# Kernel optimization log

Hardware: AMD Instinct MI355X
Metric: run time of the kernel (lower is better)

## Reference

```python
import jax, jax.numpy as jnp
import numpy as np

B, H, E = 1024, 2048, 1024

def _xavier(key, shape):
    # torch xavier_normal_ on [1, out, in]: std = sqrt(2/(fan_in+fan_out)) over last two dims
    fan_out, fan_in = shape[-2], shape[-1]
    std = (2.0 / (fan_in + fan_out)) ** 0.5
    return jax.random.normal(key, shape, jnp.float32) * std

def setup_inputs() -> dict:
    key = jax.random.key(0)
    ks = jax.random.split(key, 17)
    inp = {
        'x': jax.random.normal(ks[0], (B, E, 1), jnp.float32),
        'c': jax.random.normal(ks[1], (B, H, 1), jnp.float32),
        'h': jax.random.normal(ks[2], (B, H, 1), jnp.float32),
        'W_xi': _xavier(ks[3], (1, H, E)), 'W_hi': _xavier(ks[4], (1, H, H)), 'B_i': _xavier(ks[5], (1, H, 1)),
        'W_xg': _xavier(ks[6], (1, H, E)), 'W_hg': _xavier(ks[7], (1, H, H)), 'B_g': _xavier(ks[8], (1, H, 1)),
        'W_xf': _xavier(ks[9], (1, H, E)), 'W_hf': _xavier(ks[10], (1, H, H)), 'B_f': _xavier(ks[11], (1, H, 1)),
        'W_xo': _xavier(ks[12], (1, H, E)), 'W_ho': _xavier(ks[13], (1, H, H)), 'B_o': _xavier(ks[14], (1, H, 1)),
        'W_hy': _xavier(ks[15], (1, E, H)), 'B_y': _xavier(ks[16], (1, E, 1)),
    }
    return inp

def reference(x, c, h, W_xi, W_hi, B_i, W_xg, W_hg, B_g, W_xf, W_hf, B_f, W_xo, W_ho, B_o, W_hy, B_y):
    # jnp.matmul broadcasts the leading batch dim: [1,H,E] @ [B,E,1] -> [B,H,1]
    i = jax.nn.sigmoid(jnp.matmul(W_xi, x) + jnp.matmul(W_hi, h) + B_i)
    g = jnp.tanh(jnp.matmul(W_xg, x) + jnp.matmul(W_hg, h) + B_g)
    f = jax.nn.sigmoid(jnp.matmul(W_xf, x) + jnp.matmul(W_hf, h) + B_f)
    c_new = f * c + i * g
    o = jax.nn.sigmoid(jnp.matmul(W_xo, x) + jnp.matmul(W_ho, h) + B_o)
    h_new = o * c_new  # NOTE: source uses o*c (no tanh), faithful to original
    y = jnp.tanh(jnp.matmul(W_hy, h_new) + B_y)
    return (y, c_new, h_new)
```

## Files before the change

kernel.cpp:

```cpp
#include <hip/hip_runtime.h>

#define B_SZ 1024
#define H_SZ 2048
#define E_SZ 1024

typedef float  f32x4 __attribute__((ext_vector_type(4)));
typedef short  s16x8 __attribute__((ext_vector_type(8)));

__device__ __forceinline__ unsigned short f2bf(float f) {
    unsigned u = __float_as_uint(f);
    u = u + 0x7fffu + ((u >> 16) & 1u);
    return (unsigned short)(u >> 16);
}
__device__ __forceinline__ float bf2f(unsigned short s) {
    return __uint_as_float(((unsigned)s) << 16);
}
__device__ __forceinline__ float sigm(float v) {
    return 1.0f / (1.0f + __expf(-v));
}

__device__ __forceinline__ void gll(const unsigned short* g, unsigned short* l) {
    __builtin_amdgcn_global_load_lds(
        (const __attribute__((address_space(1))) unsigned int*)g,
        (__attribute__((address_space(3))) unsigned int*)l, 16, 0, 0);
}

struct CastArgs {
    const float*    src[11];
    unsigned short* dst[11];
    int             n[11];
};

__global__ __launch_bounds__(256) void cast_kernel(CastArgs a) {
    const int arr = blockIdx.y;
    const int n = a.n[arr];
    const float* __restrict__ s = a.src[arr];
    unsigned short* __restrict__ d = a.dst[arr];
    const int stride = gridDim.x * 256 * 4;
    for (int i = (blockIdx.x * 256 + threadIdx.x) * 4; i < n; i += stride) {
        float4 v = *(const float4*)(s + i);
        ushort4 o;
        o.x = f2bf(v.x); o.y = f2bf(v.y); o.z = f2bf(v.z); o.w = f2bf(v.w);
        *(ushort4*)(d + i) = o;
    }
}

__device__ __forceinline__ void gemm_accum64(
    const unsigned short* __restrict__ A,
    const unsigned short* __restrict__ W,
    int ld, int kLen, int m0, int n0,
    unsigned short* lA, unsigned short* lB,
    f32x4 acc[4][4], int t)
{
    const int lane = t & 63;
    const int w    = t >> 6;
    const int wr   = (w >> 1) << 6;
    const int wc   = (w & 1) << 6;
    const int lr   = lane & 15;
    const int q4   = lane >> 4;

    const int srow = t >> 3;
    const int scol = ((t & 7) ^ (srow & 7)) << 3;
    const unsigned short* gA = A + (size_t)(m0 + srow) * ld + scol;
    const unsigned short* gB = W + (size_t)(n0 + srow) * ld + scol;
    const size_t st32 = (size_t)32 * ld;

    const int cb0 = ((q4    ) ^ (lr & 7)) << 3;
    const int cb1 = ((4 + q4) ^ (lr & 7)) << 3;

    for (int k0 = 0; k0 < kLen; k0 += 64) {
#pragma unroll
        for (int p = 0; p < 4; ++p)
            gll(gA + k0 + p * st32, lA + (t + 256 * p) * 8);
#pragma unroll
        for (int p = 0; p < 4; ++p)
            gll(gB + k0 + p * st32, lB + (t + 256 * p) * 8);
        __syncthreads();

#pragma unroll
        for (int ks = 0; ks < 2; ++ks) {
            const int cb = ks ? cb1 : cb0;
            s16x8 af[4], bfr[4];
#pragma unroll
            for (int i = 0; i < 4; ++i)
                af[i] = *(const s16x8*)(lA + (wr + i * 16 + lr) * 64 + cb);
#pragma unroll
            for (int j = 0; j < 4; ++j)
                bfr[j] = *(const s16x8*)(lB + (wc + j * 16 + lr) * 64 + cb);
#pragma unroll
            for (int i = 0; i < 4; ++i)
#pragma unroll
                for (int j = 0; j < 4; ++j)
                    acc[i][j] = __builtin_amdgcn_mfma_f32_16x16x32_bf16(
                        af[i], bfr[j], acc[i][j], 0, 0, 0);
        }
        __syncthreads();
    }
}

__global__ __launch_bounds__(256) void gates_kernel(
    const unsigned short* __restrict__ Xb,
    const unsigned short* __restrict__ Hb,
    const unsigned short* __restrict__ Wxb,
    const unsigned short* __restrict__ Whb,
    const float* __restrict__ bi, const float* __restrict__ bg,
    const float* __restrict__ bff, const float* __restrict__ bo,
    unsigned short* __restrict__ Z)
{
    __shared__ unsigned short lA[128 * 64];
    __shared__ unsigned short lB[128 * 64];
    const int t   = threadIdx.x;
    const int b   = blockIdx.x;
    const int xcd = b & 7;
    const int i_  = b >> 3;
    const int nt  = xcd * 8 + (i_ >> 3);
    const int m0  = (i_ & 7) * 128;
    const int q   = nt >> 4;
    const int n0  = (nt & 15) * 128;

    f32x4 acc[4][4] = {};
    gemm_accum64(Xb, Wxb + (size_t)q * H_SZ * E_SZ, E_SZ, E_SZ, m0, n0, lA, lB, acc, t);
    gemm_accum64(Hb, Whb + (size_t)q * H_SZ * H_SZ, H_SZ, H_SZ, m0, n0, lA, lB, acc, t);

    const float* bias = (q == 0) ? bi : (q == 1) ? bg : (q == 2) ? bff : bo;
    const int lane = t & 63, w = t >> 6;
    const int wr = (w >> 1) << 6, wc = (w & 1) << 6;
    const int lr = lane & 15, rq = (lane >> 4) << 2;
    unsigned short* Zq = Z + (size_t)q * B_SZ * H_SZ;
#pragma unroll
    for (int i = 0; i < 4; ++i) {
#pragma unroll
        for (int j = 0; j < 4; ++j) {
            const int n = n0 + wc + j * 16 + lr;
            const float bv = bias[n];
#pragma unroll
            for (int r = 0; r < 4; ++r) {
                const int m = m0 + wr + i * 16 + rq + r;
                const float v = acc[i][j][r] + bv;
                const float a = (q == 1) ? tanhf(v) : sigm(v);
                Zq[(size_t)m * H_SZ + n] = f2bf(a);
            }
        }
    }
}

__global__ __launch_bounds__(256) void cell_kernel(
    const unsigned short* __restrict__ Z, const float* __restrict__ c,
    float* __restrict__ c_out, float* __restrict__ h_out,
    unsigned short* __restrict__ HnB)
{
    const size_t BH = (size_t)B_SZ * H_SZ;
    const int idx = (blockIdx.x * 256 + threadIdx.x) * 4;
    ushort4 iu = *(const ushort4*)(Z + idx);
    ushort4 gu = *(const ushort4*)(Z + BH + idx);
    ushort4 fu = *(const ushort4*)(Z + 2 * BH + idx);
    ushort4 ou = *(const ushort4*)(Z + 3 * BH + idx);
    float4 cv = *(const float4*)(c + idx);

    float cn[4], hn[4];
    cn[0] = bf2f(fu.x) * cv.x + bf2f(iu.x) * bf2f(gu.x);
    cn[1] = bf2f(fu.y) * cv.y + bf2f(iu.y) * bf2f(gu.y);
    cn[2] = bf2f(fu.z) * cv.z + bf2f(iu.z) * bf2f(gu.z);
    cn[3] = bf2f(fu.w) * cv.w + bf2f(iu.w) * bf2f(gu.w);
    hn[0] = bf2f(ou.x) * cn[0];
    hn[1] = bf2f(ou.y) * cn[1];
    hn[2] = bf2f(ou.z) * cn[2];
    hn[3] = bf2f(ou.w) * cn[3];

    *(float4*)(c_out + idx) = make_float4(cn[0], cn[1], cn[2], cn[3]);
    *(float4*)(h_out + idx) = make_float4(hn[0], hn[1], hn[2], hn[3]);
    ushort4 hb;
    hb.x = f2bf(hn[0]); hb.y = f2bf(hn[1]); hb.z = f2bf(hn[2]); hb.w = f2bf(hn[3]);
    *(ushort4*)(HnB + idx) = hb;
}

__global__ __launch_bounds__(256) void y_split_kernel(
    const unsigned short* __restrict__ Hn,
    const unsigned short* __restrict__ Wy,
    float* __restrict__ part)
{
    __shared__ unsigned short lA[128 * 64];
    __shared__ unsigned short lB[128 * 64];
    const int t   = threadIdx.x;
    const int b   = blockIdx.x;
    const int xcd = b & 7;
    const int i_  = b >> 3;
    const int ns  = xcd * 4 + (i_ >> 3);
    const int m0  = (i_ & 7) * 128;
    const int n0  = (ns >> 2) * 128;
    const int s   = ns & 3;

    f32x4 acc[4][4] = {};
    gemm_accum64(Hn + s * 512, Wy + s * 512, H_SZ, 512, m0, n0, lA, lB, acc, t);

    const int lane = t & 63, w = t >> 6;
    const int wr = (w >> 1) << 6, wc = (w & 1) << 6;
    const int lr = lane & 15, rq = (lane >> 4) << 2;
    float* P = part + (size_t)s * B_SZ * E_SZ;
#pragma unroll
    for (int i = 0; i < 4; ++i) {
#pragma unroll
        for (int j = 0; j < 4; ++j) {
            const int n = n0 + wc + j * 16 + lr;
#pragma unroll
            for (int r = 0; r < 4; ++r) {
                const int m = m0 + wr + i * 16 + rq + r;
                P[(size_t)m * E_SZ + n] = acc[i][j][r];
            }
        }
    }
}

__global__ __launch_bounds__(256) void y_reduce_kernel(
    const float* __restrict__ part, const float* __restrict__ by,
    float* __restrict__ yout)
{
    const size_t BE = (size_t)B_SZ * E_SZ;
    const int idx = (blockIdx.x * 256 + threadIdx.x) * 4;
    float4 a = *(const float4*)(part + idx);
    float4 b2 = *(const float4*)(part + BE + idx);
    float4 c2 = *(const float4*)(part + 2 * BE + idx);
    float4 d2 = *(const float4*)(part + 3 * BE + idx);
    const int col = idx & (E_SZ - 1);
    float4 bv = *(const float4*)(by + col);
    float4 o;
    o.x = tanhf(a.x + b2.x + c2.x + d2.x + bv.x);
    o.y = tanhf(a.y + b2.y + c2.y + d2.y + bv.y);
    o.z = tanhf(a.z + b2.z + c2.z + d2.z + bv.z);
    o.w = tanhf(a.w + b2.w + c2.w + d2.w + bv.w);
    *(float4*)(yout + idx) = o;
}

extern "C" void kernel_launch(void* const* d_in, const int* in_sizes, int n_in,
                              void* d_out, int out_size, void* d_ws, size_t ws_size,
                              hipStream_t stream) {
    const float* x   = (const float*)d_in[0];
    const float* c   = (const float*)d_in[1];
    const float* h   = (const float*)d_in[2];
    const float* Wxi = (const float*)d_in[3];
    const float* Whi = (const float*)d_in[4];
    const float* Bi  = (const float*)d_in[5];
    const float* Wxg = (const float*)d_in[6];
    const float* Whg = (const float*)d_in[7];
    const float* Bg  = (const float*)d_in[8];
    const float* Wxf = (const float*)d_in[9];
    const float* Whf = (const float*)d_in[10];
    const float* Bf  = (const float*)d_in[11];
    const float* Wxo = (const float*)d_in[12];
    const float* Who = (const float*)d_in[13];
    const float* Bo  = (const float*)d_in[14];
    const float* Why = (const float*)d_in[15];
    const float* By  = (const float*)d_in[16];

    const size_t BE = (size_t)B_SZ * E_SZ, BH = (size_t)B_SZ * H_SZ;
    const size_t HE = (size_t)H_SZ * E_SZ, HH = (size_t)H_SZ * H_SZ;
    const size_t EH = (size_t)E_SZ * H_SZ;

    unsigned short* ws   = (unsigned short*)d_ws;
    unsigned short* Xb   = ws;
    unsigned short* Hb   = Xb + BE;
    unsigned short* Wxb  = Hb + BH;
    unsigned short* Whb  = Wxb + 4 * HE;
    unsigned short* Whyb = Whb + 4 * HH;
    unsigned short* Z    = Whyb + EH;
    unsigned short* HnB  = Z + 4 * BH;

    CastArgs ca;
    ca.src[0]  = x;   ca.dst[0]  = Xb;           ca.n[0]  = (int)BE;
    ca.src[1]  = h;   ca.dst[1]  = Hb;           ca.n[1]  = (int)BH;
    ca.src[2]  = Wxi; ca.dst[2]  = Wxb;          ca.n[2]  = (int)HE;
    ca.src[3]  = Wxg; ca.dst[3]  = Wxb + HE;     ca.n[3]  = (int)HE;
    ca.src[4]  = Wxf; ca.dst[4]  = Wxb + 2 * HE; ca.n[4]  = (int)HE;
    ca.src[5]  = Wxo; ca.dst[5]  = Wxb + 3 * HE; ca.n[5]  = (int)HE;
    ca.src[6]  = Whi; ca.dst[6]  = Whb;          ca.n[6]  = (int)HH;
    ca.src[7]  = Whg; ca.dst[7]  = Whb + HH;     ca.n[7]  = (int)HH;
    ca.src[8]  = Whf; ca.dst[8]  = Whb + 2 * HH; ca.n[8]  = (int)HH;
    ca.src[9]  = Who; ca.dst[9]  = Whb + 3 * HH; ca.n[9]  = (int)HH;
    ca.src[10] = Why; ca.dst[10] = Whyb;         ca.n[10] = (int)EH;

    hipLaunchKernelGGL(cast_kernel, dim3(1024, 11), dim3(256), 0, stream, ca);
    hipLaunchKernelGGL(gates_kernel, dim3(512), dim3(256), 0, stream,
                       Xb, Hb, Wxb, Whb, Bi, Bg, Bf, Bo, Z);

    float* y_out = (float*)d_out;
    float* c_out = y_out + BE;
    float* h_out = c_out + BH;
    hipLaunchKernelGGL(cell_kernel, dim3((unsigned)(BH / 1024)), dim3(256), 0, stream,
                       Z, c, c_out, h_out, HnB);

    float* ypart = (float*)Z;
    hipLaunchKernelGGL(y_split_kernel, dim3(256), dim3(256), 0, stream,
                       HnB, Whyb, ypart);
    hipLaunchKernelGGL(y_reduce_kernel, dim3((unsigned)(BE / 1024)), dim3(256), 0, stream,
                       ypart, By, y_out);
}
```

Baseline: 268.1 us.

## Rewrite gates GEMM with 256x128 tiles and a pipelined, swizzled LDS loop

Replaces the 128x128 gates GEMM with a 512-thread kernel that computes a 256x128 tile, so the grid shrinks to 256 blocks. It fuses the x and h K-loops into one 48-step loop that prefetches ahead into double-buffered LDS halves through global_load_lds. LDS is XOR-swizzled to reduce bank conflicts, and the loop uses explicit waitcnt/barrier ordering with s_setprio around the MFMA bursts. The aim is to hide global load latency behind compute and raise per-CU arithmetic intensity. The cost is a large LDS footprint (about 96KB) and hand-tuned synchronization that depends on exact vmcnt counts.

```diff
diff --git a/kernel.cpp b/kernel.cpp
--- a/kernel.cpp
+++ b/kernel.cpp
@@ -98,7 +98,9 @@
     }
 }
 
-__global__ __launch_bounds__(256) void gates_kernel(
+#define GNT 48
+
+__global__ __launch_bounds__(512, 2) void gates8_kernel(
     const unsigned short* __restrict__ Xb,
     const unsigned short* __restrict__ Hb,
     const unsigned short* __restrict__ Wxb,
@@ -107,36 +109,130 @@
     const float* __restrict__ bff, const float* __restrict__ bo,
     unsigned short* __restrict__ Z)
 {
-    __shared__ unsigned short lA[128 * 64];
-    __shared__ unsigned short lB[128 * 64];
+    __shared__ unsigned short lA[4 * 8192];
+    __shared__ unsigned short lB[4 * 4096];
+
     const int t   = threadIdx.x;
     const int b   = blockIdx.x;
     const int xcd = b & 7;
     const int i_  = b >> 3;
-    const int nt  = xcd * 8 + (i_ >> 3);
-    const int m0  = (i_ & 7) * 128;
-    const int q   = nt >> 4;
-    const int n0  = (nt & 15) * 128;
+    const int ntg = xcd * 8 + (i_ >> 2);
+    const int m0  = (i_ & 3) * 256;
+    const int n0g = ntg * 128;
+    const int q   = n0g >> 11;
+    const int nl  = n0g & (H_SZ - 1);
+
+    const int sc = (((t & 3) ^ ((t >> 3) & 3)) << 3);
+    const int rA = t >> 2;
+    const unsigned short* AE0 = Xb + (size_t)(m0 + rA) * E_SZ + sc;
+    const unsigned short* AE1 = AE0 + (size_t)128 * E_SZ;
+    const unsigned short* AH0 = Hb + (size_t)(m0 + rA) * H_SZ + sc;
+    const unsigned short* AH1 = AH0 + (size_t)128 * H_SZ;
+    const unsigned short* BEp = Wxb + (size_t)q * H_SZ * E_SZ + (size_t)(nl + rA) * E_SZ + sc;
+    const unsigned short* BHp = Whb + (size_t)q * H_SZ * H_SZ + (size_t)(nl + rA) * H_SZ + sc;
+
+    auto stageA = [&](int s, int kh) {
+        unsigned short* d = lA + ((((s & 1) << 1) + kh) << 13) + t * 8;
+        if (s < 16) { const int k = s * 64 + kh * 32;        gll(AE0 + k, d); gll(AE1 + k, d + 4096); }
+        else        { const int k = (s - 16) * 64 + kh * 32; gll(AH0 + k, d); gll(AH1 + k, d + 4096); }
+    };
+    auto stageB = [&](int s, int kh) {
+        unsigned short* d = lB + ((((s & 1) << 1) + kh) << 12) + t * 8;
+        if (s < 16) gll(BEp + s * 64 + kh * 32, d);
+        else        gll(BHp + (s - 16) * 64 + kh * 32, d);
+    };
+
+    stageA(0, 0); stageB(0, 0);
+    stageA(0, 1); stageB(0, 1);
+    stageA(1, 0); stageB(1, 0);
+
+    const int lane = t & 63;
+    const int w    = t >> 6;
+    const int wr   = (w >> 1) << 6;
+    const int wc   = (w & 1) << 6;
+    const int lr   = lane & 15;
+    const int q4   = lane >> 4;
+    int offA[4], offB[4];
+#pragma unroll
+    for (int i = 0; i < 4; ++i) {
+        const int ra = wr + i * 16 + lr;
+        offA[i] = ra * 32 + ((q4 ^ ((ra >> 1) & 3)) << 3);
+        const int rb = wc + i * 16 + lr;
+        offB[i] = rb * 32 + ((q4 ^ ((rb >> 1) & 3)) << 3);
+    }
 
     f32x4 acc[4][4] = {};
-    gemm_accum64(Xb, Wxb + (size_t)q * H_SZ * E_SZ, E_SZ, E_SZ, m0, n0, lA, lB, acc, t);
-    gemm_accum64(Hb, Whb + (size_t)q * H_SZ * H_SZ, H_SZ, H_SZ, m0, n0, lA, lB, acc, t);
+
+    asm volatile("s_waitcnt vmcnt(6)" ::: "memory");
+    asm volatile("s_barrier" ::: "memory");
+
+    for (int tt = 0; tt < GNT; ++tt) {
+        const int bufb = (tt & 1) << 1;
+        {
+            const unsigned short* pA = lA + ((bufb + 0) << 13);
+            const unsigned short* pB = lB + ((bufb + 0) << 12);
+            s16x8 af[4], bv[4];
+#pragma unroll
+            for (int i = 0; i < 4; ++i) af[i] = *(const s16x8*)(pA + offA[i]);
+#pragma unroll
+            for (int j = 0; j < 4; ++j) bv[j] = *(const s16x8*)(pB + offB[j]);
+            if (tt + 1 < GNT) { stageA(tt + 1, 1); stageB(tt + 1, 1); }
+            asm volatile("s_barrier" ::: "memory");
+            asm volatile("s_waitcnt lgkmcnt(0)" ::: "memory");
+            __builtin_amdgcn_sched_barrier(0);
+            __builtin_amdgcn_s_setprio(1);
+#pragma unroll
+            for (int i = 0; i < 4; ++i)
+#pragma unroll
+                for (int j = 0; j < 4; ++j)
+                    acc[i][j] = __builtin_amdgcn_mfma_f32_16x16x32_bf16(
+                        af[i], bv[j], acc[i][j], 0, 0, 0);
+            __builtin_amdgcn_sched_barrier(0);
+            __builtin_amdgcn_s_setprio(0);
+            if (tt + 1 < GNT) asm volatile("s_waitcnt vmcnt(6)" ::: "memory");
+            else              asm volatile("s_waitcnt vmcnt(0)" ::: "memory");
+            asm volatile("s_barrier" ::: "memory");
+        }
+        {
+            const unsigned short* pA = lA + ((bufb + 1) << 13);
+            const unsigned short* pB = lB + ((bufb + 1) << 12);
+            s16x8 af[4], bv[4];
+#pragma unroll
+            for (int i = 0; i < 4; ++i) af[i] = *(const s16x8*)(pA + offA[i]);
+#pragma unroll
+            for (int j = 0; j < 4; ++j) bv[j] = *(const s16x8*)(pB + offB[j]);
+            if (tt + 2 < GNT) { stageA(tt + 2, 0); stageB(tt + 2, 0); }
+            asm volatile("s_barrier" ::: "memory");
+            asm volatile("s_waitcnt lgkmcnt(0)" ::: "memory");
+            __builtin_amdgcn_sched_barrier(0);
+            __builtin_amdgcn_s_setprio(1);
+#pragma unroll
+            for (int i = 0; i < 4; ++i)
+#pragma unroll
+                for (int j = 0; j < 4; ++j)
+                    acc[i][j] = __builtin_amdgcn_mfma_f32_16x16x32_bf16(
+                        af[i], bv[j], acc[i][j], 0, 0, 0);
+            __builtin_amdgcn_sched_barrier(0);
+            __builtin_amdgcn_s_setprio(0);
+            if (tt + 2 < GNT)      asm volatile("s_waitcnt vmcnt(6)" ::: "memory");
+            else if (tt + 1 < GNT) asm volatile("s_waitcnt vmcnt(3)" ::: "memory");
+            asm volatile("s_barrier" ::: "memory");
+        }
+    }
 
     const float* bias = (q == 0) ? bi : (q == 1) ? bg : (q == 2) ? bff : bo;
-    const int lane = t & 63, w = t >> 6;
-    const int wr = (w >> 1) << 6, wc = (w & 1) << 6;
-    const int lr = lane & 15, rq = (lane >> 4) << 2;
     unsigned short* Zq = Z + (size_t)q * B_SZ * H_SZ;
+    const int rq = (lane >> 4) << 2;
 #pragma unroll
     for (int i = 0; i < 4; ++i) {
 #pragma unroll
         for (int j = 0; j < 4; ++j) {
-            const int n = n0 + wc + j * 16 + lr;
-            const float bv = bias[n];
+            const int n = nl + wc + j * 16 + lr;
+            const float bvv = bias[n];
 #pragma unroll
             for (int r = 0; r < 4; ++r) {
                 const int m = m0 + wr + i * 16 + rq + r;
-                const float v = acc[i][j][r] + bv;
+                const float v = acc[i][j][r] + bvv;
                 const float a = (q == 1) ? tanhf(v) : sigm(v);
                 Zq[(size_t)m * H_SZ + n] = f2bf(a);
             }
@@ -279,7 +375,7 @@
     ca.src[10] = Why; ca.dst[10] = Whyb;         ca.n[10] = (int)EH;
 
     hipLaunchKernelGGL(cast_kernel, dim3(1024, 11), dim3(256), 0, stream, ca);
-    hipLaunchKernelGGL(gates_kernel, dim3(512), dim3(256), 0, stream,
+    hipLaunchKernelGGL(gates8_kernel, dim3(256), dim3(512), 0, stream,
                        Xb, Hb, Wxb, Whb, Bi, Bg, Bf, Bo, Z);
 
     float* y_out = (float*)d_out;
```

Result: slower. 278.1 us (+3.7%).

## Rewrite gates GEMM with 256x128 tiles and a 6-stage async LDS pipeline

Applied to the files above, without the earlier changes.

Replaces the gates GEMM with a 512-thread kernel that computes 256x128 output tiles, one block per CU. K-slices of 32 are streamed into six LDS buffers with global_load_lds, kept several stages ahead, and synchronised with explicit vmcnt waits and barriers. An XOR swizzle on the LDS column chunk avoids bank conflicts, and setprio raises priority around the MFMA bursts. The goal is to hide global-load latency and raise MFMA use, at the cost of about 144KB of LDS per block, which allows only one block per CU.

```diff
diff --git a/kernel.cpp b/kernel.cpp
--- a/kernel.cpp
+++ b/kernel.cpp
@@ -98,7 +98,7 @@
     }
 }
 
-__global__ __launch_bounds__(256) void gates_kernel(
+__global__ __launch_bounds__(512, 2) void gates8_kernel(
     const unsigned short* __restrict__ Xb,
     const unsigned short* __restrict__ Hb,
     const unsigned short* __restrict__ Wxb,
@@ -107,36 +107,119 @@
     const float* __restrict__ bff, const float* __restrict__ bo,
     unsigned short* __restrict__ Z)
 {
-    __shared__ unsigned short lA[128 * 64];
-    __shared__ unsigned short lB[128 * 64];
+    __shared__ unsigned short lA[6 * 8192];
+    __shared__ unsigned short lB[6 * 4096];
+
     const int t   = threadIdx.x;
     const int b   = blockIdx.x;
     const int xcd = b & 7;
     const int i_  = b >> 3;
-    const int nt  = xcd * 8 + (i_ >> 3);
-    const int m0  = (i_ & 7) * 128;
-    const int q   = nt >> 4;
-    const int n0  = (nt & 15) * 128;
+    const int ntg = xcd * 8 + (i_ >> 2);
+    const int m0  = (i_ & 3) * 256;
+    const int n0g = ntg * 128;
+    const int q   = n0g >> 11;
+    const int nl  = n0g & (H_SZ - 1);
+
+    const int sc = (((t & 3) ^ ((t >> 3) & 3)) << 3);
+    const int rA = t >> 2;
+    const unsigned short* AE0 = Xb + (size_t)(m0 + rA) * E_SZ + sc;
+    const unsigned short* AE1 = AE0 + (size_t)128 * E_SZ;
+    const unsigned short* AH0 = Hb + (size_t)(m0 + rA) * H_SZ + sc;
+    const unsigned short* AH1 = AH0 + (size_t)128 * H_SZ;
+    const unsigned short* BEp = Wxb + (size_t)q * H_SZ * E_SZ + (size_t)(nl + rA) * E_SZ + sc;
+    const unsigned short* BHp = Whb + (size_t)q * H_SZ * H_SZ + (size_t)(nl + rA) * H_SZ + sc;
+
+    auto stage = [&](int h, unsigned short* dA, unsigned short* dB) {
+        if (h < 32) {
+            const int k = h * 32;
+            gll(AE0 + k, dA); gll(AE1 + k, dA + 4096); gll(BEp + k, dB);
+        } else {
+            const int k = (h - 32) * 32;
+            gll(AH0 + k, dA); gll(AH1 + k, dA + 4096); gll(BHp + k, dB);
+        }
+    };
+
+    const int lane = t & 63;
+    const int w    = t >> 6;
+    const int wr   = (w >> 1) << 6;
+    const int wc   = (w & 1) << 6;
+    const int lr   = lane & 15;
+    const int q4   = lane >> 4;
+    int offA[4], offB[4];
+#pragma unroll
+    for (int i = 0; i < 4; ++i) {
+        const int ra = wr + i * 16 + lr;
+        offA[i] = ra * 32 + ((q4 ^ ((ra >> 1) & 3)) << 3);
+        const int rb = wc + i * 16 + lr;
+        offB[i] = rb * 32 + ((q4 ^ ((rb >> 1) & 3)) << 3);
+    }
 
     f32x4 acc[4][4] = {};
-    gemm_accum64(Xb, Wxb + (size_t)q * H_SZ * E_SZ, E_SZ, E_SZ, m0, n0, lA, lB, acc, t);
-    gemm_accum64(Hb, Whb + (size_t)q * H_SZ * H_SZ, H_SZ, H_SZ, m0, n0, lA, lB, acc, t);
+
+    stage(0, lA + 0 * 8192 + t * 8, lB + 0 * 4096 + t * 8);
+    stage(1, lA + 1 * 8192 + t * 8, lB + 1 * 4096 + t * 8);
+    stage(2, lA + 2 * 8192 + t * 8, lB + 2 * 4096 + t * 8);
+    stage(3, lA + 3 * 8192 + t * 8, lB + 3 * 4096 + t * 8);
+    asm volatile("s_waitcnt vmcnt(9)" ::: "memory");
+    asm volatile("s_barrier" ::: "memory");
+
+#define PHASE(P_, S, SN, WAITN, DO_STAGE)                                 \
+  {                                                                       \
+    const unsigned short* pA = lA + (S) * 8192;                           \
+    const unsigned short* pB = lB + (S) * 4096;                           \
+    s16x8 af[4], bv[4];                                                   \
+    af[0] = *(const s16x8*)(pA + offA[0]);                                \
+    af[1] = *(const s16x8*)(pA + offA[1]);                                \
+    af[2] = *(const s16x8*)(pA + offA[2]);                                \
+    af[3] = *(const s16x8*)(pA + offA[3]);                                \
+    bv[0] = *(const s16x8*)(pB + offB[0]);                                \
+    bv[1] = *(const s16x8*)(pB + offB[1]);                                \
+    bv[2] = *(const s16x8*)(pB + offB[2]);                                \
+    bv[3] = *(const s16x8*)(pB + offB[3]);                                \
+    if (DO_STAGE) stage((P_) + 4, lA + (SN) * 8192 + t * 8,               \
+                        lB + (SN) * 4096 + t * 8);                        \
+    asm volatile("s_waitcnt vmcnt(" WAITN ")" ::: "memory");              \
+    asm volatile("s_barrier" ::: "memory");                               \
+    asm volatile("s_waitcnt lgkmcnt(0)" ::: "memory");                    \
+    __builtin_amdgcn_sched_barrier(0);                                    \
+    __builtin_amdgcn_s_setprio(1);                                        \
+    _Pragma("unroll") for (int i2 = 0; i2 < 4; ++i2)                      \
+      _Pragma("unroll") for (int j2 = 0; j2 < 4; ++j2)                    \
+        acc[i2][j2] = __builtin_amdgcn_mfma_f32_16x16x32_bf16(            \
+            af[i2], bv[j2], acc[i2][j2], 0, 0, 0);                        \
+    __builtin_amdgcn_s_setprio(0);                                        \
+  }
+
+    for (int g = 0; g < 15; ++g) {
+        const int h0 = g * 6;
+        PHASE(h0 + 0, 0, 4, "9", true);
+        PHASE(h0 + 1, 1, 5, "9", true);
+        PHASE(h0 + 2, 2, 0, "9", true);
+        PHASE(h0 + 3, 3, 1, "9", true);
+        PHASE(h0 + 4, 4, 2, "9", true);
+        PHASE(h0 + 5, 5, 3, "9", true);
+    }
+    PHASE(90, 0, 4, "9", true);
+    PHASE(91, 1, 5, "9", true);
+    PHASE(92, 2, 0, "6", false);
+    PHASE(93, 3, 1, "3", false);
+    PHASE(94, 4, 2, "0", false);
+    PHASE(95, 5, 3, "0", false);
+#undef PHASE
 
     const float* bias = (q == 0) ? bi : (q == 1) ? bg : (q == 2) ? bff : bo;
-    const int lane = t & 63, w = t >> 6;
-    const int wr = (w >> 1) << 6, wc = (w & 1) << 6;
-    const int lr = lane & 15, rq = (lane >> 4) << 2;
     unsigned short* Zq = Z + (size_t)q * B_SZ * H_SZ;
+    const int rq = (lane >> 4) << 2;
 #pragma unroll
     for (int i = 0; i < 4; ++i) {
 #pragma unroll
         for (int j = 0; j < 4; ++j) {
-            const int n = n0 + wc + j * 16 + lr;
-            const float bv = bias[n];
+            const int n = nl + wc + j * 16 + lr;
+            const float bvv = bias[n];
 #pragma unroll
             for (int r = 0; r < 4; ++r) {
                 const int m = m0 + wr + i * 16 + rq + r;
-                const float v = acc[i][j][r] + bv;
+                const float v = acc[i][j][r] + bvv;
                 const float a = (q == 1) ? tanhf(v) : sigm(v);
                 Zq[(size_t)m * H_SZ + n] = f2bf(a);
             }
@@ -279,7 +362,7 @@
     ca.src[10] = Why; ca.dst[10] = Whyb;         ca.n[10] = (int)EH;
 
     hipLaunchKernelGGL(cast_kernel, dim3(1024, 11), dim3(256), 0, stream, ca);
-    hipLaunchKernelGGL(gates_kernel, dim3(512), dim3(256), 0, stream,
+    hipLaunchKernelGGL(gates8_kernel, dim3(256), dim3(512), 0, stream,
                        Xb, Hb, Wxb, Whb, Bi, Bg, Bf, Bo, Z);
 
     float* y_out = (float*)d_out;
```

Result: slower. 325.2 us (+21.3%).

## Fuse fp32-to-bf16 weight conversion into GEMM tile loads, drop weight cast pass

Applied to the files above, without the earlier changes.

Weights are no longer cast to bf16 in a separate pass over all 11 matrices. Each GEMM tile loop instead loads fp32 weight rows into registers, packs them with v_cvt_pk_bf16_f32 and writes them to LDS, while activations still use direct global-to-LDS loads. This removes a full read and write of about 50M weight elements. The cost is that the GEMMs read fp32 weights at twice the bytes, and the register-staged loads are not overlapped with compute. The packed conversion may also round differently from the old software f2bf.

```diff
diff --git a/kernel.cpp b/kernel.cpp
--- a/kernel.cpp
+++ b/kernel.cpp
@@ -18,6 +18,11 @@
 __device__ __forceinline__ float sigm(float v) {
     return 1.0f / (1.0f + __expf(-v));
 }
+__device__ __forceinline__ unsigned cvtpk(float lo, float hi) {
+    unsigned r;
+    asm("v_cvt_pk_bf16_f32 %0, %1, %2" : "=v"(r) : "v"(lo), "v"(hi));
+    return r;
+}
 
 __device__ __forceinline__ void gll(const unsigned short* g, unsigned short* l) {
     __builtin_amdgcn_global_load_lds(
@@ -26,9 +31,9 @@
 }
 
 struct CastArgs {
-    const float*    src[11];
-    unsigned short* dst[11];
-    int             n[11];
+    const float*    src[2];
+    unsigned short* dst[2];
+    int             n[2];
 };
 
 __global__ __launch_bounds__(256) void cast_kernel(CastArgs a) {
@@ -45,9 +50,9 @@
     }
 }
 
-__device__ __forceinline__ void gemm_accum64(
+__device__ __forceinline__ void gemm_accum64_bf32(
     const unsigned short* __restrict__ A,
-    const unsigned short* __restrict__ W,
+    const float* __restrict__ W,
     int ld, int kLen, int m0, int n0,
     unsigned short* lA, unsigned short* lB,
     f32x4 acc[4][4], int t)
@@ -62,19 +67,32 @@
     const int srow = t >> 3;
     const int scol = ((t & 7) ^ (srow & 7)) << 3;
     const unsigned short* gA = A + (size_t)(m0 + srow) * ld + scol;
-    const unsigned short* gB = W + (size_t)(n0 + srow) * ld + scol;
+    const float*          gB = W + (size_t)(n0 + srow) * ld + scol;
     const size_t st32 = (size_t)32 * ld;
 
     const int cb0 = ((q4    ) ^ (lr & 7)) << 3;
     const int cb1 = ((4 + q4) ^ (lr & 7)) << 3;
 
     for (int k0 = 0; k0 < kLen; k0 += 64) {
+        float4 f[4][2];
+#pragma unroll
+        for (int p = 0; p < 4; ++p) {
+            const float* src = gB + k0 + p * st32;
+            f[p][0] = *(const float4*)(src);
+            f[p][1] = *(const float4*)(src + 4);
+        }
 #pragma unroll
         for (int p = 0; p < 4; ++p)
             gll(gA + k0 + p * st32, lA + (t + 256 * p) * 8);
 #pragma unroll
-        for (int p = 0; p < 4; ++p)
-            gll(gB + k0 + p * st32, lB + (t + 256 * p) * 8);
+        for (int p = 0; p < 4; ++p) {
+            uint4 pk;
+            pk.x = cvtpk(f[p][0].x, f[p][0].y);
+            pk.y = cvtpk(f[p][0].z, f[p][0].w);
+            pk.z = cvtpk(f[p][1].x, f[p][1].y);
+            pk.w = cvtpk(f[p][1].z, f[p][1].w);
+            *(uint4*)(lB + (t + 256 * p) * 8) = pk;
+        }
         __syncthreads();
 
 #pragma unroll
@@ -98,15 +116,13 @@
     }
 }
 
-__global__ __launch_bounds__(256) void gates_kernel(
-    const unsigned short* __restrict__ Xb,
-    const unsigned short* __restrict__ Hb,
-    const unsigned short* __restrict__ Wxb,
-    const unsigned short* __restrict__ Whb,
-    const float* __restrict__ bi, const float* __restrict__ bg,
-    const float* __restrict__ bff, const float* __restrict__ bo,
-    unsigned short* __restrict__ Z)
-{
+struct GatesArgs {
+    const unsigned short *Xb, *Hb;
+    const float *Wx[4], *Wh[4], *bias[4];
+    unsigned short *Z;
+};
+
+__global__ __launch_bounds__(256) void gates_kernel(GatesArgs a) {
     __shared__ unsigned short lA[128 * 64];
     __shared__ unsigned short lB[128 * 64];
     const int t   = threadIdx.x;
@@ -119,14 +135,14 @@
     const int n0  = (nt & 15) * 128;
 
     f32x4 acc[4][4] = {};
-    gemm_accum64(Xb, Wxb + (size_t)q * H_SZ * E_SZ, E_SZ, E_SZ, m0, n0, lA, lB, acc, t);
-    gemm_accum64(Hb, Whb + (size_t)q * H_SZ * H_SZ, H_SZ, H_SZ, m0, n0, lA, lB, acc, t);
-
-    const float* bias = (q == 0) ? bi : (q == 1) ? bg : (q == 2) ? bff : bo;
+    gemm_accum64_bf32(a.Xb, a.Wx[q], E_SZ, E_SZ, m0, n0, lA, lB, acc, t);
+    gemm_accum64_bf32(a.Hb, a.Wh[q], H_SZ, H_SZ, m0, n0, lA, lB, acc, t);
+
+    const float* bias = a.bias[q];
     const int lane = t & 63, w = t >> 6;
     const int wr = (w >> 1) << 6, wc = (w & 1) << 6;
     const int lr = lane & 15, rq = (lane >> 4) << 2;
-    unsigned short* Zq = Z + (size_t)q * B_SZ * H_SZ;
+    unsigned short* Zq = a.Z + (size_t)q * B_SZ * H_SZ;
 #pragma unroll
     for (int i = 0; i < 4; ++i) {
 #pragma unroll
@@ -137,8 +153,8 @@
             for (int r = 0; r < 4; ++r) {
                 const int m = m0 + wr + i * 16 + rq + r;
                 const float v = acc[i][j][r] + bv;
-                const float a = (q == 1) ? tanhf(v) : sigm(v);
-                Zq[(size_t)m * H_SZ + n] = f2bf(a);
+                const float act = (q == 1) ? tanhf(v) : sigm(v);
+                Zq[(size_t)m * H_SZ + n] = f2bf(act);
             }
         }
     }
@@ -176,7 +192,7 @@
 
 __global__ __launch_bounds__(256) void y_split_kernel(
     const unsigned short* __restrict__ Hn,
-    const unsigned short* __restrict__ Wy,
+    const float* __restrict__ Wy,
     float* __restrict__ part)
 {
     __shared__ unsigned short lA[128 * 64];
@@ -191,7 +207,7 @@
     const int s   = ns & 3;
 
     f32x4 acc[4][4] = {};
-    gemm_accum64(Hn + s * 512, Wy + s * 512, H_SZ, 512, m0, n0, lA, lB, acc, t);
+    gemm_accum64_bf32(Hn + s * 512, Wy + s * 512, H_SZ, 512, m0, n0, lA, lB, acc, t);
 
     const int lane = t & 63, w = t >> 6;
     const int wr = (w >> 1) << 6, wc = (w & 1) << 6;
@@ -253,34 +269,25 @@
     const float* By  = (const float*)d_in[16];
 
     const size_t BE = (size_t)B_SZ * E_SZ, BH = (size_t)B_SZ * H_SZ;
-    const size_t HE = (size_t)H_SZ * E_SZ, HH = (size_t)H_SZ * H_SZ;
-    const size_t EH = (size_t)E_SZ * H_SZ;
-
-    unsigned short* ws   = (unsigned short*)d_ws;
-    unsigned short* Xb   = ws;
-    unsigned short* Hb   = Xb + BE;
-    unsigned short* Wxb  = Hb + BH;
-    unsigned short* Whb  = Wxb + 4 * HE;
-    unsigned short* Whyb = Whb + 4 * HH;
-    unsigned short* Z    = Whyb + EH;
-    unsigned short* HnB  = Z + 4 * BH;
+
+    unsigned short* ws  = (unsigned short*)d_ws;
+    unsigned short* Xb  = ws;
+    unsigned short* Hb  = Xb + BE;
+    unsigned short* Z   = Hb + BH;
+    unsigned short* HnB = Z + 4 * BH;
 
     CastArgs ca;
-    ca.src[0]  = x;   ca.dst[0]  = Xb;           ca.n[0]  = (int)BE;
-    ca.src[1]  = h;   ca.dst[1]  = Hb;           ca.n[1]  = (int)BH;
-    ca.src[2]  = Wxi; ca.dst[2]  = Wxb;          ca.n[2]  = (int)HE;
-    ca.src[3]  = Wxg; ca.dst[3]  = Wxb + HE;     ca.n[3]  = (int)HE;
-    ca.src[4]  = Wxf; ca.dst[4]  = Wxb + 2 * HE; ca.n[4]  = (int)HE;
-    ca.src[5]  = Wxo; ca.dst[5]  = Wxb + 3 * HE; ca.n[5]  = (int)HE;
-    ca.src[6]  = Whi; ca.dst[6]  = Whb;          ca.n[6]  = (int)HH;
-    ca.src[7]  = Whg; ca.dst[7]  = Whb + HH;     ca.n[7]  = (int)HH;
-    ca.src[8]  = Whf; ca.dst[8]  = Whb + 2 * HH; ca.n[8]  = (int)HH;
-    ca.src[9]  = Who; ca.dst[9]  = Whb + 3 * HH; ca.n[9]  = (int)HH;
-    ca.src[10] = Why; ca.dst[10] = Whyb;         ca.n[10] = (int)EH;
-
-    hipLaunchKernelGGL(cast_kernel, dim3(1024, 11), dim3(256), 0, stream, ca);
-    hipLaunchKernelGGL(gates_kernel, dim3(512), dim3(256), 0, stream,
-                       Xb, Hb, Wxb, Whb, Bi, Bg, Bf, Bo, Z);
+    ca.src[0] = x; ca.dst[0] = Xb; ca.n[0] = (int)BE;
+    ca.src[1] = h; ca.dst[1] = Hb; ca.n[1] = (int)BH;
+    hipLaunchKernelGGL(cast_kernel, dim3(512, 2), dim3(256), 0, stream, ca);
+
+    GatesArgs ga;
+    ga.Xb = Xb; ga.Hb = Hb;
+    ga.Wx[0] = Wxi; ga.Wx[1] = Wxg; ga.Wx[2] = Wxf; ga.Wx[3] = Wxo;
+    ga.Wh[0] = Whi; ga.Wh[1] = Whg; ga.Wh[2] = Whf; ga.Wh[3] = Who;
+    ga.bias[0] = Bi; ga.bias[1] = Bg; ga.bias[2] = Bf; ga.bias[3] = Bo;
+    ga.Z = Z;
+    hipLaunchKernelGGL(gates_kernel, dim3(512), dim3(256), 0, stream, ga);
 
     float* y_out = (float*)d_out;
     float* c_out = y_out + BE;
@@ -290,7 +297,7 @@
 
     float* ypart = (float*)Z;
     hipLaunchKernelGGL(y_split_kernel, dim3(256), dim3(256), 0, stream,
-                       HnB, Whyb, ypart);
+                       HnB, Why, ypart);
     hipLaunchKernelGGL(y_reduce_kernel, dim3((unsigned)(BE / 1024)), dim3(256), 0, stream,
                        ypart, By, y_out);
 }
```

Measured after the change: 282.1 us. 5.2% more time.
